# Performance work log

Measured on AMD Instinct MI355X. Metric: run time of the kernel, lower is better.

## Reference

```python
import jax, jax.numpy as jnp
import numpy as np

N = 20000        # nodes
E = 320000       # edges (avg degree 16)
G = 128          # graphs in batch
D_IN = 128
H = 128          # hidden_dim
HEADS = 8
OUT = 2
BN_EPS = 1e-5


def _segment_softmax(logits, seg, num_segments):
    # numerically stable softmax over segments along leading dim
    m = jax.ops.segment_max(logits, seg, num_segments)
    e = jnp.exp(logits - m[seg])
    s = jax.ops.segment_sum(e, seg, num_segments)
    return e / (s[seg] + 1e-16)


def _forward(x, gin1_w1, gin1_b1, gin1_w2, gin1_b2,
             gin2_w1, gin2_b1, gin2_w2, gin2_b2,
             gin3_w1, gin3_b1, gin3_w2, gin3_b2,
             gin4_w1, gin4_b1, gin4_w2, gin4_b2,
             bn1_g, bn1_b, bn2_g, bn2_b, bn3_g, bn3_b, bn4_g, bn4_b, bn5_g, bn5_b,
             gat_w, gat_asrc, gat_adst, gat_bias,
             gate_w, gate_b, fc1_w, fc1_b, fc2_w, fc2_b,
             edge_index, batch):
    src, dst = edge_index[0], edge_index[1]

    def gin(h, w1, b1, w2, b2):
        # GINConv, eps=0: mlp(x + sum_{j->i} x_j)
        agg = jax.ops.segment_sum(h[src], dst, N)
        z = agg + h
        return jax.nn.relu(z @ w1 + b1) @ w2 + b2

    def bn(h, g, b):
        # BatchNorm1d with batch statistics (training-mode normalization)
        mu = h.mean(0)
        var = ((h - mu) ** 2).mean(0)
        return g * (h - mu) * jax.lax.rsqrt(var + BN_EPS) + b

    # dropout is identity at inference
    h = jax.nn.relu(bn(gin(x, gin1_w1, gin1_b1, gin1_w2, gin1_b2), bn1_g, bn1_b))
    h = jax.nn.relu(bn(gin(h, gin2_w1, gin2_b1, gin2_w2, gin2_b2), bn2_g, bn2_b))
    h = jax.nn.relu(bn(gin(h, gin3_w1, gin3_b1, gin3_w2, gin3_b2), bn3_g, bn3_b))
    h = jax.nn.relu(bn(gin(h, gin4_w1, gin4_b1, gin4_w2, gin4_b2), bn4_g, bn4_b))

    # GATConv(2H -> H, heads=HEADS, concat=False) with self-loops (PyG default)
    loop = jnp.arange(N)
    s = jnp.concatenate([src, loop])
    d = jnp.concatenate([dst, loop])
    xh = (h @ gat_w).reshape(N, HEADS, H)                     # [N, heads, H]
    a_s = jnp.einsum('nhc,hc->nh', xh, gat_asrc)              # [N, heads]
    a_d = jnp.einsum('nhc,hc->nh', xh, gat_adst)
    e = jax.nn.leaky_relu(a_s[s] + a_d[d], 0.2)               # [E+N, heads]
    alpha = _segment_softmax(e, d, N)                         # softmax over in-edges of dst
    out = jax.ops.segment_sum(alpha[:, :, None] * xh[s], d, N)  # [N, heads, H]
    h = out.mean(1) + gat_bias                                # concat=False -> mean heads
    h = jax.nn.relu(bn(h, bn5_g, bn5_b))

    # GlobalAttention pooling: softmax(gate_nn(x)) per graph, weighted sum
    gate_logit = (h @ gate_w + gate_b)[:, 0]                  # [N]
    gate = _segment_softmax(gate_logit, batch, G)
    pooled = jax.ops.segment_sum(gate[:, None] * h, batch, G)  # [G, H]

    return jax.nn.relu(pooled @ fc1_w + fc1_b) @ fc2_w + fc2_b  # [G, OUT]


def setup_inputs() -> dict:
    key = jax.random.key(0)
    kit = iter(jax.random.split(key, 64))

    def nrm(shape, s=0.05):
        return jax.random.normal(next(kit), shape, jnp.float32) * s

    inp = {}
    inp['x'] = jax.random.normal(next(kit), (N, D_IN), jnp.float32)
    inp['edge_index'] = jax.random.randint(next(kit), (2, E), 0, N)
    inp['batch'] = jnp.sort(jax.random.randint(next(kit), (N,), 0, G))
    gin_dims = [(D_IN, H), (H, 2 * H), (2 * H, 4 * H), (4 * H, 2 * H)]
    for i, (a, b) in enumerate(gin_dims, 1):
        inp[f'gin{i}_w1'] = nrm((a, b))
        inp[f'gin{i}_b1'] = jnp.zeros((b,), jnp.float32)
        inp[f'gin{i}_w2'] = nrm((b, b))
        inp[f'gin{i}_b2'] = jnp.zeros((b,), jnp.float32)
    for i, dd in enumerate([H, 2 * H, 4 * H, 2 * H, H], 1):
        inp[f'bn{i}_g'] = jnp.ones((dd,), jnp.float32)
        inp[f'bn{i}_b'] = jnp.zeros((dd,), jnp.float32)
    inp['gat_w'] = nrm((2 * H, HEADS * H))
    inp['gat_asrc'] = nrm((HEADS, H))
    inp['gat_adst'] = nrm((HEADS, H))
    inp['gat_bias'] = jnp.zeros((H,), jnp.float32)
    inp['gate_w'] = nrm((H, 1))
    inp['gate_b'] = jnp.zeros((1,), jnp.float32)
    inp['fc1_w'] = nrm((H, 128))
    inp['fc1_b'] = jnp.zeros((128,), jnp.float32)
    inp['fc2_w'] = nrm((128, OUT))
    inp['fc2_b'] = jnp.zeros((OUT,), jnp.float32)
    return inp


def reference(x, edge_index, batch,
              gin1_w1, gin1_b1, gin1_w2, gin1_b2,
              gin2_w1, gin2_b1, gin2_w2, gin2_b2,
              gin3_w1, gin3_b1, gin3_w2, gin3_b2,
              gin4_w1, gin4_b1, gin4_w2, gin4_b2,
              bn1_g, bn1_b, bn2_g, bn2_b, bn3_g, bn3_b, bn4_g, bn4_b, bn5_g, bn5_b,
              gat_w, gat_asrc, gat_adst, gat_bias,
              gate_w, gate_b, fc1_w, fc1_b, fc2_w, fc2_b):
    return _forward(x, gin1_w1, gin1_b1, gin1_w2, gin1_b2,
                    gin2_w1, gin2_b1, gin2_w2, gin2_b2,
                    gin3_w1, gin3_b1, gin3_w2, gin3_b2,
                    gin4_w1, gin4_b1, gin4_w2, gin4_b2,
                    bn1_g, bn1_b, bn2_g, bn2_b, bn3_g, bn3_b, bn4_g, bn4_b, bn5_g, bn5_b,
                    gat_w, gat_asrc, gat_adst, gat_bias,
                    gate_w, gate_b, fc1_w, fc1_b, fc2_w, fc2_b,
                    edge_index, batch)
```

## Files before the change

kernel.cpp:

```cpp
#include <hip/hip_runtime.h>
#include <hip/hip_bf16.h>
#include <math.h>

#define NN 20000
#define NE 320000
#define NG 128

using bf16x8 = __attribute__((ext_vector_type(8))) short;
using f32x4  = __attribute__((ext_vector_type(4))) float;

static __device__ __forceinline__ float lrelu(float v){ return v > 0.f ? v : 0.2f*v; }
static __device__ __forceinline__ float b2f(unsigned short u){ unsigned int v = ((unsigned int)u) << 16; return __uint_as_float(v); }
static __device__ __forceinline__ unsigned short f2b(float f){
  unsigned int x = __float_as_uint(f);
  unsigned int r = x + 0x7fffu + ((x >> 16) & 1u);
  return (unsigned short)(r >> 16);
}
static __device__ __forceinline__ void gl16(const unsigned short* g, unsigned short* l){
  __builtin_amdgcn_global_load_lds((const __attribute__((address_space(1))) void*)g,
                                   (__attribute__((address_space(3))) void*)l, 16, 0, 0);
}
static __device__ __forceinline__ uint4 bn8(uint4 u, const float* scs, const float* shs, int f0){
  float v[8] = { b2f(u.x & 0xffff), b2f(u.x >> 16), b2f(u.y & 0xffff), b2f(u.y >> 16),
                 b2f(u.z & 0xffff), b2f(u.z >> 16), b2f(u.w & 0xffff), b2f(u.w >> 16) };
// ... 59 lines not shown
  }
}

struct WPrep {
  const float* W[9];
  unsigned short* Wt[9];
  int K[9];
  int Nn[9];
  int tileStart[10];
  const float* x;
  unsigned int* xb;
};

__global__ __launch_bounds__(256)
void k_prep2(WPrep P){
  __shared__ float tile[64][65];
  int b = blockIdx.x;
  if (b < P.tileStart[9]){
    int i = 0;
    while (i < 8 && b >= P.tileStart[i+1]) i++;
    int ti = b - P.tileStart[i];
    int K = P.K[i], Nn = P.Nn[i];
    int ntc = Nn >> 6;
    int k0 = (ti / ntc) << 6, n0 = (ti % ntc) << 6;
    int c = threadIdx.x & 63, ro = threadIdx.x >> 6;
    const float* W = P.W[i];
    #pragma unroll
    for (int rr = 0; rr < 16; rr++){
      int r = rr*4 + ro;
      tile[c][r] = W[(size_t)(k0 + r)*Nn + n0 + c];
    }
    __syncthreads();
    unsigned short* Wt = P.Wt[i];
    #pragma unroll
    for (int cc = 0; cc < 16; cc++){
      int cidx = cc*4 + ro;
      Wt[(size_t)(n0 + cidx)*K + k0 + c] = f2b(tile[cidx][c]);
    }
  } else {
    int idx = (b - P.tileStart[9])*256 + threadIdx.x;
    if (idx < NN*64){
      unsigned int lo = f2b(P.x[2*idx]);
      unsigned int hi = f2b(P.x[2*idx + 1]);
      P.xb[idx] = lo | (hi << 16);
    }
  }
}

template<int MODE, int DU>
__global__ __launch_bounds__(256)
void k_agg(const unsigned int* __restrict__ hU, const int* __restrict__ ptr,
           const int* __restrict__ csrc, unsigned int* __restrict__ z,
           const double* __restrict__ stats, const float* __restrict__ g,
           const float* __restrict__ bb, const float* __restrict__ bias){
  const int d = DU*2;
  __shared__ float scs[MODE == 1 ? 512 : 1];
  __shared__ float shs[MODE == 1 ? 512 : 1];
  int t = threadIdx.x;
  if (MODE == 1){
    for (int f = t; f < d; f += 256){
      double inv = 1.0 / (double)NN;
      double mu  = stats[f]*inv;
      double var = stats[d + f]*inv - mu*mu;
      if (var < 0.0) var = 0.0;
      float sc = g[f] * rsqrtf((float)var + 1e-5f);
      scs[f] = sc;
      shs[f] = bb[f] - (float)mu*sc;
    }
    __syncthreads();
  }
  const int npb = 256/DU;
  int n  = blockIdx.x*npb + t/DU;
  int tl = t & (DU - 1);
  int f0 = 2*tl, f1 = f0 + 1;
  float sc0 = 0.f, sh0 = 0.f, sc1 = 0.f, sh1 = 0.f;
  if (MODE == 1){ sc0 = scs[f0]; sh0 = shs[f0]; sc1 = scs[f1]; sh1 = shs[f1]; }
  int beg = ptr[n], deg = ptr[n+1] - beg;
  unsigned int self = hU[(size_t)n*DU + tl];
  float a0, a1;
// ... 7 lines not shown
  int i = 0;
  for (; i + 8 <= deg; i += 8){
    unsigned int v[8];
    #pragma unroll
    for (int u = 0; u < 8; u++) v[u] = hU[(size_t)csrc[beg + i + u]*DU + tl];
    #pragma unroll
    for (int u = 0; u < 8; u++){
      if (MODE == 1){
        a0 += fmaxf(b2f(v[u] & 0xffff)*sc0 + sh0, 0.f);
        a1 += fmaxf(b2f(v[u] >> 16)   *sc1 + sh1, 0.f);
      } else {
        a0 += b2f(v[u] & 0xffff);
        a1 += b2f(v[u] >> 16);
      }
    }
  }
  for (; i < deg; i++){
    unsigned int v = hU[(size_t)csrc[beg + i]*DU + tl];
    if (MODE == 1){
      a0 += fmaxf(b2f(v & 0xffff)*sc0 + sh0, 0.f);
      a1 += fmaxf(b2f(v >> 16)   *sc1 + sh1, 0.f);
    } else {
      a0 += b2f(v & 0xffff);
      a1 += b2f(v >> 16);
    }
  }
  if (MODE == 2){
    a0 = fmaxf(a0 + bias[f0], 0.f);
    a1 = fmaxf(a1 + bias[f1], 0.f);
  }
  z[(size_t)n*DU + tl] = (unsigned int)f2b(a0) | ((unsigned int)f2b(a1) << 16);
}

template<int ACT, int OBF, int STATS, int SCORES, int BNA>
__global__ __launch_bounds__(256)
void k_gemm_mfma(const unsigned short* __restrict__ A, const unsigned short* __restrict__ Bt,
                 const float* __restrict__ bias, float* __restrict__ C,
                 unsigned short* __restrict__ Cb, double* __restrict__ stats,
                 const float* __restrict__ asrc, const float* __restrict__ adst,
                 float* __restrict__ a_s, float* __restrict__ a_d,
                 const double* __restrict__ bnst, const float* __restrict__ bng,
                 const float* __restrict__ bnb,
                 int M, int Nn, int K){
  const int LDA = BNA ? 40 : 32;
  __shared__ unsigned short As[2][128*(BNA ? 40 : 32)];
  __shared__ unsigned short Bs[2][128*32];
  __shared__ float sS[SCORES ? 128 : 1];
  __shared__ float sD[SCORES ? 128 : 1];
  __shared__ float scs[BNA ? 512 : 1];
  __shared__ float shs[BNA ? 512 : 1];
  const int bm = blockIdx.y*128, bn = blockIdx.x*128;
  const int tid = threadIdx.x;
  const int lane = tid & 63;
  const int wave = tid >> 6;
  const int wm = (wave >> 1)*64, wn = (wave & 1)*64;
  const int lr = lane & 15, lq = lane >> 4;

  f32x4 acc[4][4];
  #pragma unroll
  for (int i = 0; i < 4; i++)
    #pragma unroll
    for (int j = 0; j < 4; j++) acc[i][j] = (f32x4){0.f,0.f,0.f,0.f};

  const int rowA = tid >> 2, q = tid & 3;
  const int ldsOff = wave*16*32;
  const int gmA0 = min(bm + rowA,      M-1);
  const int gmA1 = min(bm + rowA + 64, M-1);
  const unsigned short* pA0 = &A[(size_t)gmA0*K + q*8];
  const unsigned short* pA1 = &A[(size_t)gmA1*K + q*8];
  const unsigned short* pB0 = &Bt[(size_t)(bn + rowA)*K + q*8];
  const unsigned short* pB1 = &Bt[(size_t)(bn + rowA + 64)*K + q*8];

  if (BNA){
    for (int f = tid; f < K; f += 256){
      double inv = 1.0 / (double)NN;
      double mu  = bnst[f]*inv;
      double var = bnst[K + f]*inv - mu*mu;
      if (var < 0.0) var = 0.0;
      float sc = bng[f] * rsqrtf((float)var + 1e-5f);
      scs[f] = sc;
      shs[f] = bnb[f] - (float)mu*sc;
// ... 33 lines not shown
    bf16x8 af[4], bf[4];
    #pragma unroll
    for (int mi = 0; mi < 4; mi++)
      af[mi] = *(const bf16x8*)&As[cur][(wm + mi*16 + lr)*LDA + lq*8];
    #pragma unroll
    for (int ni = 0; ni < 4; ni++)
      bf[ni] = *(const bf16x8*)&Bs[cur][(wn + ni*16 + lr)*32 + lq*8];
    #pragma unroll
    for (int mi = 0; mi < 4; mi++)
      #pragma unroll
      for (int ni = 0; ni < 4; ni++)
        acc[mi][ni] = __builtin_amdgcn_mfma_f32_16x16x32_bf16(af[mi], bf[ni], acc[mi][ni], 0, 0, 0);
    if (BNA && kn < K){
      int f0 = kn + q*8;
      *(uint4*)&As[cur^1][ rowA      *LDA + q*8] = bn8(nu0, scs, shs, f0);
      *(uint4*)&As[cur^1][(rowA + 64)*LDA + q*8] = bn8(nu1, scs, shs, f0);
    }
    __syncthreads();
    cur ^= 1;
  }

  float cs[4] = {0.f,0.f,0.f,0.f}, cq[4] = {0.f,0.f,0.f,0.f};
  #pragma unroll
  for (int mi = 0; mi < 4; mi++){
    #pragma unroll
    for (int j = 0; j < 4; j++){
      int gm = bm + wm + mi*16 + lq*4 + j;
      if (gm < M){
        #pragma unroll
        for (int ni = 0; ni < 4; ni++){
          int gn = bn + wn + ni*16 + lr;
          float v = acc[mi][ni][j] + (bias ? bias[gn] : 0.f);
          if (ACT) v = fmaxf(v, 0.f);
          if (OBF) Cb[(size_t)gm*Nn + gn] = f2b(v);
          else     C [(size_t)gm*Nn + gn] = v;
          if (STATS){ cs[ni] += v; cq[ni] += v*v; }
        }
      }
    }
  }
  if (STATS){
    #pragma unroll
    for (int ni = 0; ni < 4; ni++){
      float s = cs[ni], qq = cq[ni];
      s += __shfl_xor(s, 16); s += __shfl_xor(s, 32);
      qq += __shfl_xor(qq, 16); qq += __shfl_xor(qq, 32);
      if (lane < 16){
        int gn = bn + wn + ni*16 + lr;
        atomicAdd(&stats[gn],      (double)s);
        atomicAdd(&stats[Nn + gn], (double)qq);
      }
    }
  }
  if (SCORES){
    const int hd = bn >> 7;
    float av[4], dv[4];
    #pragma unroll
    for (int ni = 0; ni < 4; ni++){
      int c = wn + ni*16 + lr;
      av[ni] = asrc[hd*128 + c];
      dv[ni] = adst[hd*128 + c];
    }
    float psS[4][4], psD[4][4];
    #pragma unroll
    for (int mi = 0; mi < 4; mi++)
      #pragma unroll
      for (int j = 0; j < 4; j++){
        float s = 0.f, d2 = 0.f;
        #pragma unroll
        for (int ni = 0; ni < 4; ni++){
          float v = acc[mi][ni][j];
          s  += v*av[ni];
          d2 += v*dv[ni];
        }
        #pragma unroll
        for (int o = 1; o < 16; o <<= 1){ s += __shfl_xor(s, o); d2 += __shfl_xor(d2, o); }
        psS[mi][j] = s; psD[mi][j] = d2;
      }
    if (wn == 0 && lr == 0){
      #pragma unroll
      for (int mi = 0; mi < 4; mi++)
        #pragma unroll
        for (int j = 0; j < 4; j++){
          int r = wm + mi*16 + lq*4 + j;
          sS[r] = psS[mi][j]; sD[r] = psD[mi][j];
        }
    }
    __syncthreads();
    if (wn != 0 && lr == 0){
      #pragma unroll
      for (int mi = 0; mi < 4; mi++)
        #pragma unroll
        for (int j = 0; j < 4; j++){
          int r = wm + mi*16 + lq*4 + j;
          sS[r] += psS[mi][j]; sD[r] += psD[mi][j];
        }
    }
    __syncthreads();
    if (tid < 128){
      int gm = bm + tid;
      if (gm < M){ a_s[gm*8 + hd] = sS[tid]; a_d[gm*8 + hd] = sD[tid]; }
    }
  }
}

__global__ __launch_bounds__(256)
void k_gin1_mlp(const unsigned short* __restrict__ Z, const unsigned short* __restrict__ W1t,
                const float* __restrict__ b1, const unsigned short* __restrict__ W2t,
                const float* __restrict__ b2, unsigned short* __restrict__ Out,
                double* __restrict__ stats, int M){
  __shared__ unsigned short As[2][128*32];
  __shared__ unsigned short Bs[2][128*32];
  __shared__ unsigned short hid[128*136];
  const int bm = blockIdx.x*128;
  const int tid = threadIdx.x;
  const int lane = tid & 63;
  const int wave = tid >> 6;
  const int wm = (wave >> 1)*64, wn = (wave & 1)*64;
  const int lr = lane & 15, lq = lane >> 4;
  const int rowA = tid >> 2, q = tid & 3;
  const int ldsOff = wave*16*32;
  const int gm0 = min(bm + rowA,      M-1);
  const int gm1 = min(bm + rowA + 64, M-1);
  const unsigned short* pA0 = &Z[(size_t)gm0*128 + q*8];
  const unsigned short* pA1 = &Z[(size_t)gm1*128 + q*8];
  const unsigned short* pB0 = &W1t[(size_t)rowA*128 + q*8];
  const unsigned short* pB1 = &W1t[(size_t)(rowA + 64)*128 + q*8];

  f32x4 acc[4][4];
  #pragma unroll
  for (int i = 0; i < 4; i++)
    #pragma unroll
    for (int j = 0; j < 4; j++) acc[i][j] = (f32x4){0.f,0.f,0.f,0.f};

// ... 76 lines not shown
    __syncthreads();
    cur ^= 1;
  }
  float cs[4] = {0.f,0.f,0.f,0.f}, cq[4] = {0.f,0.f,0.f,0.f};
  #pragma unroll
  for (int mi = 0; mi < 4; mi++){
    #pragma unroll
    for (int j = 0; j < 4; j++){
      int gm = bm + wm + mi*16 + lq*4 + j;
      if (gm < M){
        #pragma unroll
        for (int ni = 0; ni < 4; ni++){
          int gn = wn + ni*16 + lr;
          float v = acc2[mi][ni][j] + b2[gn];
          Out[(size_t)gm*128 + gn] = f2b(v);
          cs[ni] += v; cq[ni] += v*v;
        }
      }
    }
  }
  #pragma unroll
  for (int ni = 0; ni < 4; ni++){
    float s = cs[ni], qq = cq[ni];
    s += __shfl_xor(s, 16); s += __shfl_xor(s, 32);
    qq += __shfl_xor(qq, 16); qq += __shfl_xor(qq, 32);
    if (lane < 16){
      int gn = wn + ni*16 + lr;
      atomicAdd(&stats[gn],       (double)s);
      atomicAdd(&stats[128 + gn], (double)qq);
    }
  }
}

__global__ void k_bn_stats16(const unsigned short* __restrict__ h, int d, double* __restrict__ stats){
  int r0 = blockIdx.x*64;
  int rend = min(NN, r0 + 64);
  for (int f = threadIdx.x; f < d; f += blockDim.x){
    float s = 0.f, q = 0.f;
    for (int r = r0; r < rend; r++){ float v = b2f(h[(size_t)r*d + f]); s += v; q += v*v; }
    atomicAdd(&stats[f], (double)s);
    atomicAdd(&stats[d + f], (double)q);
  }
}

__global__ __launch_bounds__(256)
void k_bn_relu_gate(const unsigned short* __restrict__ hpre, unsigned short* __restrict__ hb,
                    int total8, const double* __restrict__ stats,
                    const float* __restrict__ g, const float* __restrict__ b,
                    const float* __restrict__ gatew, const float* __restrict__ gateb,
                    float* __restrict__ logit){
  const int d = 128;
  __shared__ float scs[128], shs[128];
  for (int f = threadIdx.x; f < d; f += blockDim.x){
    double inv = 1.0 / (double)NN;
    double mu  = stats[f]*inv;
    double var = stats[d + f]*inv - mu*mu;
    if (var < 0.0) var = 0.0;
    float sc = g[f] * rsqrtf((float)var + 1e-5f);
    scs[f] = sc;
    shs[f] = b[f] - (float)mu*sc;
  }
  __syncthreads();
  int i = blockIdx.x*blockDim.x + threadIdx.x;
  if (i >= total8) return;
  int i8 = i*8;
  uint4 u = *(const uint4*)&hpre[i8];
  float v[8] = { b2f(u.x & 0xffff), b2f(u.x >> 16), b2f(u.y & 0xffff), b2f(u.y >> 16),
                 b2f(u.z & 0xffff), b2f(u.z >> 16), b2f(u.w & 0xffff), b2f(u.w >> 16) };
  int f0 = i8 & 127;
  float gp = 0.f;
  #pragma unroll
  for (int j = 0; j < 8; j++){
    float y = fmaxf(v[j]*scs[f0 + j] + shs[f0 + j], 0.f);
    v[j] = y;
    gp += y*gatew[f0 + j];
  }
  uint4 p;
  p.x = (unsigned int)f2b(v[0]) | ((unsigned int)f2b(v[1]) << 16);
  p.y = (unsigned int)f2b(v[2]) | ((unsigned int)f2b(v[3]) << 16);
  p.z = (unsigned int)f2b(v[4]) | ((unsigned int)f2b(v[5]) << 16);
  p.w = (unsigned int)f2b(v[6]) | ((unsigned int)f2b(v[7]) << 16);
  *(uint4*)&hb[i8] = p;
  #pragma unroll
  for (int o = 1; o < 16; o <<= 1) gp += __shfl_xor(gp, o);
  if ((threadIdx.x & 15) == 0) logit[i >> 4] = gp + gateb[0];
}

__global__ __launch_bounds__(256)
void k_gat_node256(const unsigned short* __restrict__ xh, const float* __restrict__ a_s,
                   const float* __restrict__ a_d, const int* __restrict__ ptr,
                   const int* __restrict__ csrc, const float* __restrict__ bias,
                   unsigned short* __restrict__ hout){
  int n = blockIdx.x, t = threadIdx.x;
  int beg = ptr[n], deg = ptr[n+1] - beg;
  int tot = deg + 1;
  __shared__ float elv[256][9];
  __shared__ int esrc[256];
  __shared__ float red[256];
  __shared__ float ms[8], ssinv[8], adn[8];
  __shared__ float partial[16][132];
  if (t < 8) adn[t] = a_d[n*8 + t];
  __syncthreads();
  int head = t >> 5, slot = t & 31;
  int sub = t >> 7, tt = t & 127;
  int h16 = tt >> 4;
  float acc[8] = {0.f,0.f,0.f,0.f,0.f,0.f,0.f,0.f};

  if (tot <= 256){
    for (int i = t; i < tot; i += 256) esrc[i] = (i < deg) ? csrc[beg + i] : n;
    __syncthreads();
    for (int i = t; i < tot*8; i += 256){
      int le = i >> 3, hh = i & 7;
      elv[le][hh] = lrelu(a_s[esrc[le]*8 + hh] + adn[hh]);
    }
    __syncthreads();
    float mx = -1e30f;
    for (int e = slot; e < tot; e += 32) mx = fmaxf(mx, elv[e][head]);
    red[t] = mx; __syncthreads();
    #pragma unroll
    for (int off = 16; off >= 1; off >>= 1){
      if (slot < off) red[t] = fmaxf(red[t], red[t + off]);
      __syncthreads();
    }
    if (slot == 0) ms[head] = red[t];
    __syncthreads();
    float sm = 0.f;
    for (int e = slot; e < tot; e += 32){
      float ex = __expf(elv[e][head] - ms[head]);
      elv[e][head] = ex;
      sm += ex;
    }
    red[t] = sm; __syncthreads();
    #pragma unroll
    for (int off = 16; off >= 1; off >>= 1){
      if (slot < off) red[t] += red[t + off];
      __syncthreads();
    }
    if (slot == 0) ssinv[head] = 1.f / (red[t] + 1e-16f);
    __syncthreads();
    int lo = sub*128, hi = min(tot, lo + 128);
    float si = ssinv[h16];
    int i = lo;
    for (; i + 2 <= hi; i += 2){
      const uint4* r0 = (const uint4*)(xh + (size_t)esrc[i]*1024);
      const uint4* r1 = (const uint4*)(xh + (size_t)esrc[i+1]*1024);
      uint4 v0 = r0[tt], v1 = r1[tt];
      float a0 = elv[i][h16]*si, a1 = elv[i+1][h16]*si;
      acc[0] += a0*b2f(v0.x & 0xffff) + a1*b2f(v1.x & 0xffff);
      acc[1] += a0*b2f(v0.x >> 16)    + a1*b2f(v1.x >> 16);
      acc[2] += a0*b2f(v0.y & 0xffff) + a1*b2f(v1.y & 0xffff);
      acc[3] += a0*b2f(v0.y >> 16)    + a1*b2f(v1.y >> 16);
      acc[4] += a0*b2f(v0.z & 0xffff) + a1*b2f(v1.z & 0xffff);
      acc[5] += a0*b2f(v0.z >> 16)    + a1*b2f(v1.z >> 16);
      acc[6] += a0*b2f(v0.w & 0xffff) + a1*b2f(v1.w & 0xffff);
      acc[7] += a0*b2f(v0.w >> 16)    + a1*b2f(v1.w >> 16);
    }
    for (; i < hi; i++){
      const uint4* r0 = (const uint4*)(xh + (size_t)esrc[i]*1024);
      uint4 v0 = r0[tt];
      float a0 = elv[i][h16]*si;
      acc[0] += a0*b2f(v0.x & 0xffff); acc[1] += a0*b2f(v0.x >> 16);
      acc[2] += a0*b2f(v0.y & 0xffff); acc[3] += a0*b2f(v0.y >> 16);
      acc[4] += a0*b2f(v0.z & 0xffff); acc[5] += a0*b2f(v0.z >> 16);
      acc[6] += a0*b2f(v0.w & 0xffff); acc[7] += a0*b2f(v0.w >> 16);
    }
    __syncthreads();
  } else {
    float mx = -1e30f;
    for (int e = slot; e < tot; e += 32){
      int s = (e < deg) ? csrc[beg + e] : n;
      mx = fmaxf(mx, lrelu(a_s[s*8 + head] + adn[head]));
    }
    red[t] = mx; __syncthreads();
    #pragma unroll
    for (int off = 16; off >= 1; off >>= 1){
      if (slot < off) red[t] = fmaxf(red[t], red[t + off]);
      __syncthreads();
    }
    if (slot == 0) ms[head] = red[t];
    __syncthreads();
    float sm = 0.f;
    for (int e = slot; e < tot; e += 32){
      int s = (e < deg) ? csrc[beg + e] : n;
      sm += __expf(lrelu(a_s[s*8 + head] + adn[head]) - ms[head]);
    }
    red[t] = sm; __syncthreads();
    #pragma unroll
    for (int off = 16; off >= 1; off >>= 1){
      if (slot < off) red[t] += red[t + off];
      __syncthreads();
    }
    if (slot == 0) ssinv[head] = 1.f / (red[t] + 1e-16f);
    __syncthreads();
    float si = ssinv[h16];
    for (int ch = 0; ch < tot; ch += 256){
      int ce = min(256, tot - ch);
      for (int i = t; i < ce*8; i += 256){
        int le = i >> 3, hh = i & 7;
        int s = (ch + le < deg) ? csrc[beg + ch + le] : n;
        if (hh == 0) esrc[le] = s;
        elv[le][hh] = __expf(lrelu(a_s[s*8 + hh] + adn[hh]) - ms[hh]);
      }
      __syncthreads();
      int lo = sub*128, hi = min(ce, lo + 128);
      for (int i = lo; i < hi; i++){
        const uint4* r0 = (const uint4*)(xh + (size_t)esrc[i]*1024);
        uint4 v0 = r0[tt];
        float a0 = elv[i][h16]*si;
        acc[0] += a0*b2f(v0.x & 0xffff); acc[1] += a0*b2f(v0.x >> 16);
        acc[2] += a0*b2f(v0.y & 0xffff); acc[3] += a0*b2f(v0.y >> 16);
        acc[4] += a0*b2f(v0.z & 0xffff); acc[5] += a0*b2f(v0.z >> 16);
        acc[6] += a0*b2f(v0.w & 0xffff); acc[7] += a0*b2f(v0.w >> 16);
      }
      __syncthreads();
    }
  }

  int c0 = (tt & 15)*8;
  #pragma unroll
  for (int j = 0; j < 8; j++) partial[sub*8 + h16][c0 + j] = acc[j];
  __syncthreads();
  if (t < 128){
    float s = 0.f;
    #pragma unroll
    for (int g = 0; g < 16; g++) s += partial[g][t];
    hout[(size_t)n*128 + t] = f2b(s*0.125f + bias[t]);
  }
}

__global__ void k_poolhead(const unsigned short* __restrict__ h, const float* __restrict__ logit,
                           const int* __restrict__ gptr,
                           const float* __restrict__ w1, const float* __restrict__ b1,
                           const float* __restrict__ w2, const float* __restrict__ b2,
                           float* __restrict__ out){
  int g = blockIdx.x, t = threadIdx.x;
  int beg = gptr[g], end = gptr[g+1];
  __shared__ float red[128];
  __shared__ float prow[128];
  __shared__ float r1[128];
  __shared__ float m_sh, s_sh;
  float mx = -1e30f;
  for (int i = beg + t; i < end; i += 128) mx = fmaxf(mx, logit[i]);
  red[t] = mx; __syncthreads();
  for (int off = 64; off > 0; off >>= 1){ if (t < off) red[t] = fmaxf(red[t], red[t + off]); __syncthreads(); }
  if (t == 0) m_sh = red[0];
  __syncthreads();
  float sm = 0.f;
  for (int i = beg + t; i < end; i += 128) sm += __expf(logit[i] - m_sh);
  red[t] = sm; __syncthreads();
  for (int off = 64; off > 0; off >>= 1){ if (t < off) red[t] += red[t + off]; __syncthreads(); }
  if (t == 0) s_sh = red[0] + 1e-16f;
  __syncthreads();
  float acc = 0.f;
  for (int i = beg; i < end; i++){
    float w = __expf(logit[i] - m_sh) / s_sh;
    acc += w * b2f(h[(size_t)i*128 + t]);
  }
  prow[t] = acc;
  __syncthreads();
  float a = b1[t];
// ... 11 lines not shown
extern "C" void kernel_launch(void* const* d_in, const int* in_sizes, int n_in,
                              void* d_out, int out_size, void* d_ws, size_t ws_size,
                              hipStream_t stream) {
  const float* x        = (const float*)d_in[0];
  const int*   ei       = (const int*)  d_in[1];
  const int*   batch    = (const int*)  d_in[2];
  const float* gw1[4] = {(const float*)d_in[3],  (const float*)d_in[7],  (const float*)d_in[11], (const float*)d_in[15]};
  const float* gb1[4] = {(const float*)d_in[4],  (const float*)d_in[8],  (const float*)d_in[12], (const float*)d_in[16]};
  const float* gw2[4] = {(const float*)d_in[5],  (const float*)d_in[9],  (const float*)d_in[13], (const float*)d_in[17]};
  const float* gb2[4] = {(const float*)d_in[6],  (const float*)d_in[10], (const float*)d_in[14], (const float*)d_in[18]};
  const float* bng[5] = {(const float*)d_in[19], (const float*)d_in[21], (const float*)d_in[23], (const float*)d_in[25], (const float*)d_in[27]};
  const float* bnb[5] = {(const float*)d_in[20], (const float*)d_in[22], (const float*)d_in[24], (const float*)d_in[26], (const float*)d_in[28]};
  const float* gat_w    = (const float*)d_in[29];
  const float* gat_asrc = (const float*)d_in[30];
  const float* gat_adst = (const float*)d_in[31];
  const float* gat_bias = (const float*)d_in[32];
  const float* gate_w   = (const float*)d_in[33];
  const float* gate_b   = (const float*)d_in[34];
  const float* fc1_w    = (const float*)d_in[35];
  const float* fc1_b    = (const float*)d_in[36];
  const float* fc2_w    = (const float*)d_in[37];
  const float* fc2_b    = (const float*)d_in[38];
  const int* src = ei;
  const int* dst = ei + NE;

  char* wsb = (char*)d_ws;
  size_t off = 0;
  auto take = [&](size_t bytes) -> void* {
    void* p = wsb + off;
    off = (off + bytes + 255) & ~(size_t)255;
    return p;
  };
  unsigned short* hpre  = (unsigned short*)take((size_t)NN*512*2);
  unsigned short* hb    = (unsigned short*)take((size_t)NN*512*2);
  unsigned short* zh    = (unsigned short*)take((size_t)NN*1024*2);
  unsigned short* z16   = zh;
  unsigned short* hid16 = zh + (size_t)NN*512;
  unsigned short* xh16  = zh;
  unsigned short* xb    = (unsigned short*)take((size_t)NN*128*2);
  unsigned short* wt    = (unsigned short*)take((size_t)1000000*2);
  int*    deg    = (int*)   take((size_t)NN*4);
  int*    cnt    = (int*)   take((size_t)NN*4);
  int*    gdeg   = (int*)   take((size_t)NG*4);
  double* statsA = (double*)take(2560*8);
  float*  a_s    = (float*) take((size_t)NN*8*4);
  float*  a_d    = (float*) take((size_t)NN*8*4);
  float*  logit  = (float*) take((size_t)NN*4);
  int*    rowptr = (int*)   take((size_t)(NN+1)*4);
  int*    gptr   = (int*)   take((size_t)(NG+1)*4);
  int*    csrc   = (int*)   take((size_t)NE*4);
  (void)ws_size; (void)n_in; (void)in_sizes; (void)out_size;

  unsigned short* wt_g1w1 = wt;
  unsigned short* wt_g1w2 = wt_g1w1 + 128*128;
  unsigned short* wt_g2w1 = wt_g1w2 + 128*128;
  unsigned short* wt_g2w2 = wt_g2w1 + 256*128;
  unsigned short* wt_g3w1 = wt_g2w2 + 256*256;
  unsigned short* wt_g3w2 = wt_g3w1 + 512*256;
  unsigned short* wt_g4w1 = wt_g3w2 + 512*512;
  unsigned short* wt_g4w2 = wt_g4w1 + 256*512;
  unsigned short* wt_gat  = wt_g4w2 + 256*256;

  double* st1 = statsA + 0;
  double* st2 = statsA + 256;
  double* st3 = statsA + 768;
  double* st4 = statsA + 1792;
  double* st5 = statsA + 2304;

  hipMemsetAsync(deg, 0, (size_t)((char*)(statsA + 2560) - (char*)deg), stream);

  k_hist2<<<(NE + NN + 255)/256, 256, 0, stream>>>(dst, batch, deg, gdeg);
  k_scan2<<<2, 1024, 0, stream>>>(deg, rowptr, gdeg, gptr);
  k_fill<<<(NE + 255)/256, 256, 0, stream>>>(src, dst, rowptr, cnt, csrc);

  {
    WPrep P;
    const float* Ws[9] = {gw1[0], gw2[0], gw1[1], gw2[1], gw1[2], gw2[2], gw1[3], gw2[3], gat_w};
    unsigned short* Wts[9] = {wt_g1w1, wt_g1w2, wt_g2w1, wt_g2w2, wt_g3w1, wt_g3w2, wt_g4w1, wt_g4w2, wt_gat};
    int Ks[9]  = {128, 128, 128, 256, 256, 512, 512, 256, 256};
    int Nns[9] = {128, 128, 256, 256, 512, 512, 256, 256, 1024};
    int cum = 0;
    for (int i = 0; i < 9; i++){
      P.W[i] = Ws[i]; P.Wt[i] = Wts[i]; P.K[i] = Ks[i]; P.Nn[i] = Nns[i];
      P.tileStart[i] = cum;
      cum += (Ks[i] >> 6)*(Nns[i] >> 6);
    }
    P.tileStart[9] = cum;
    P.x = x; P.xb = (unsigned int*)xb;
    int xblocks = (NN*64 + 255)/256;
    k_prep2<<<cum + xblocks, 256, 0, stream>>>(P);
  }

  const int GM = (NN + 127) / 128;
  #define NP9 nullptr, nullptr, nullptr, nullptr
  #define NB3 nullptr, nullptr, nullptr

  k_agg<0,64><<<NN/4, 256, 0, stream>>>((const unsigned int*)xb, rowptr, csrc, (unsigned int*)z16, nullptr, nullptr, nullptr, nullptr);
  k_gin1_mlp<<<GM, 256, 0, stream>>>(z16, wt_g1w1, gb1[0], wt_g1w2, gb2[0], hpre, st1, NN);

  k_agg<1,64><<<NN/4, 256, 0, stream>>>((const unsigned int*)hpre, rowptr, csrc, (unsigned int*)z16, st1, bng[0], bnb[0], nullptr);
  k_gemm_mfma<1,1,0,0,0><<<dim3(2, GM), 256, 0, stream>>>(z16, wt_g2w1, gb1[1], nullptr, hid16, nullptr, NP9, NB3, NN, 256, 128);
  k_gemm_mfma<0,1,1,0,0><<<dim3(2, GM), 256, 0, stream>>>(hid16, wt_g2w2, gb2[1], nullptr, hpre, st2, NP9, NB3, NN, 256, 256);

  k_agg<1,128><<<NN/2, 256, 0, stream>>>((const unsigned int*)hpre, rowptr, csrc, (unsigned int*)z16, st2, bng[1], bnb[1], nullptr);
  k_gemm_mfma<1,1,0,0,0><<<dim3(4, GM), 256, 0, stream>>>(z16, wt_g3w1, gb1[2], nullptr, hid16, nullptr, NP9, NB3, NN, 512, 256);
  k_gemm_mfma<0,1,1,0,0><<<dim3(4, GM), 256, 0, stream>>>(hid16, wt_g3w2, gb2[2], nullptr, hpre, st3, NP9, NB3, NN, 512, 512);

  k_gemm_mfma<0,1,0,0,1><<<dim3(2, GM), 256, 0, stream>>>(hpre, wt_g4w1, nullptr, nullptr, hid16, nullptr, NP9, st3, bng[2], bnb[2], NN, 256, 512);
  k_agg<2,128><<<NN/2, 256, 0, stream>>>((const unsigned int*)hid16, rowptr, csrc, (unsigned int*)z16, nullptr, nullptr, nullptr, gb1[3]);
  k_gemm_mfma<0,1,1,0,0><<<dim3(2, GM), 256, 0, stream>>>(z16, wt_g4w2, gb2[3], nullptr, hpre, st4, NP9, NB3, NN, 256, 256);

  k_gemm_mfma<0,1,0,1,1><<<dim3(8, GM), 256, 0, stream>>>(hpre, wt_gat, nullptr, nullptr, xh16, nullptr, gat_asrc, gat_adst, a_s, a_d, st4, bng[3], bnb[3], NN, 1024, 256);
  k_gat_node256<<<NN, 256, 0, stream>>>(xh16, a_s, a_d, rowptr, csrc, gat_bias, hpre);
  k_bn_stats16<<<(NN + 63)/64, 128, 0, stream>>>(hpre, 128, st5);
  k_bn_relu_gate<<<(NN*128/8 + 255)/256, 256, 0, stream>>>(hpre, hb, NN*128/8, st5, bng[4], bnb[4], gate_w, gate_b, logit);

  k_poolhead<<<NG, 128, 0, stream>>>(hb, logit, gptr, fc1_w, fc1_b, fc2_w, fc2_b, (float*)d_out);
}
```

Measured before the change: 601.0 us.

## Reorder GAT to aggregate inputs before projection, folding attention vectors into weights

Attention scores are now computed from a small GEMM of the BN-applied input against precomputed W·a_src/W·a_dst vectors. The softmax-weighted aggregation then runs over the 256-wide input features per head. Only after that does one GEMM with a head-stacked, 1/8-scaled weight (K=2048) produce the 128-wide output, with BN stats fused into its epilogue. This avoids writing and gathering the N×1024 projected features and removes the separate BN stats kernel. In exchange the aggregation kernel writes a 2048-wide bf16 buffer per node and does 16 accumulators per thread, so memory traffic moves rather than disappearing.

Measured after the change: 617.4 us. 1.03x slower.

```diff
diff --git a/kernel.cpp b/kernel.cpp
--- a/kernel.cpp
+++ b/kernel.cpp
@@ -115,10 +115,19 @@
     }
     __syncthreads();
     unsigned short* Wt = P.Wt[i];
-    #pragma unroll
-    for (int cc = 0; cc < 16; cc++){
-      int cidx = cc*4 + ro;
-      Wt[(size_t)(n0 + cidx)*K + k0 + c] = f2b(tile[cidx][c]);
+    if (i == 8){
+      int hh = n0 >> 7, cl0 = n0 & 127;
+      #pragma unroll
+      for (int cc = 0; cc < 16; cc++){
+        int cidx = cc*4 + ro;
+        Wt[(size_t)(cl0 + cidx)*2048 + hh*256 + k0 + c] = f2b(tile[cidx][c]*0.125f);
+      }
+    } else {
+      #pragma unroll
+      for (int cc = 0; cc < 16; cc++){
+        int cidx = cc*4 + ro;
+        Wt[(size_t)(n0 + cidx)*K + k0 + c] = f2b(tile[cidx][c]);
+      }
     }
   } else {
     int idx = (b - P.tileStart[9])*256 + threadIdx.x;
@@ -128,6 +137,21 @@
       P.xb[idx] = lo | (hi << 16);
     }
   }
+}
+
+__global__ void k_wasd(const float* __restrict__ W, const float* __restrict__ asrc,
+                       const float* __restrict__ adst, unsigned short* __restrict__ Bt_sc){
+  __shared__ float av[128];
+  int b = blockIdx.x;
+  int h = b & 7, isd = b >> 3;
+  int k = threadIdx.x;
+  if (k < 128) av[k] = (isd ? adst : asrc)[h*128 + k];
+  __syncthreads();
+  const float* Wr = W + (size_t)k*1024 + h*128;
+  float s = 0.f;
+  #pragma unroll 8
+  for (int c = 0; c < 128; c++) s += Wr[c]*av[c];
+  Bt_sc[b*256 + k] = f2b(s);
 }
 
 template<int MODE, int DU>
@@ -201,21 +225,17 @@
   z[(size_t)n*DU + tl] = (unsigned int)f2b(a0) | ((unsigned int)f2b(a1) << 16);
 }
 
-template<int ACT, int OBF, int STATS, int SCORES, int BNA>
+template<int ACT, int OBF, int STATS, int PK, int BNA>
 __global__ __launch_bounds__(256)
 void k_gemm_mfma(const unsigned short* __restrict__ A, const unsigned short* __restrict__ Bt,
                  const float* __restrict__ bias, float* __restrict__ C,
                  unsigned short* __restrict__ Cb, double* __restrict__ stats,
-                 const float* __restrict__ asrc, const float* __restrict__ adst,
-                 float* __restrict__ a_s, float* __restrict__ a_d,
                  const double* __restrict__ bnst, const float* __restrict__ bng,
                  const float* __restrict__ bnb,
                  int M, int Nn, int K){
   const int LDA = BNA ? 40 : 32;
   __shared__ unsigned short As[2][128*(BNA ? 40 : 32)];
   __shared__ unsigned short Bs[2][128*32];
-  __shared__ float sS[SCORES ? 128 : 1];
-  __shared__ float sD[SCORES ? 128 : 1];
   __shared__ float scs[BNA ? 512 : 1];
   __shared__ float shs[BNA ? 512 : 1];
   const int bm = blockIdx.y*128, bn = blockIdx.x*128;
@@ -315,7 +335,8 @@
           int gn = bn + wn + ni*16 + lr;
           float v = acc[mi][ni][j] + (bias ? bias[gn] : 0.f);
           if (ACT) v = fmaxf(v, 0.f);
-          if (OBF) Cb[(size_t)gm*Nn + gn] = f2b(v);
+          if (PK){ if (gn < 16) C[(size_t)gm*16 + gn] = v; }
+          else if (OBF) Cb[(size_t)gm*Nn + gn] = f2b(v);
           else     C [(size_t)gm*Nn + gn] = v;
           if (STATS){ cs[ni] += v; cq[ni] += v*v; }
         }
@@ -333,56 +354,6 @@
         atomicAdd(&stats[gn],      (double)s);
         atomicAdd(&stats[Nn + gn], (double)qq);
       }
-    }
-  }
-  if (SCORES){
-    const int hd = bn >> 7;
-    float av[4], dv[4];
-    #pragma unroll
-    for (int ni = 0; ni < 4; ni++){
-      int c = wn + ni*16 + lr;
-      av[ni] = asrc[hd*128 + c];
-      dv[ni] = adst[hd*128 + c];
-    }
-    float psS[4][4], psD[4][4];
-    #pragma unroll
-    for (int mi = 0; mi < 4; mi++)
-      #pragma unroll
-      for (int j = 0; j < 4; j++){
-        float s = 0.f, d2 = 0.f;
-        #pragma unroll
-        for (int ni = 0; ni < 4; ni++){
-          float v = acc[mi][ni][j];
-          s  += v*av[ni];
-          d2 += v*dv[ni];
-        }
-        #pragma unroll
-        for (int o = 1; o < 16; o <<= 1){ s += __shfl_xor(s, o); d2 += __shfl_xor(d2, o); }
-        psS[mi][j] = s; psD[mi][j] = d2;
-      }
-    if (wn == 0 && lr == 0){
-      #pragma unroll
-      for (int mi = 0; mi < 4; mi++)
-        #pragma unroll
-        for (int j = 0; j < 4; j++){
-          int r = wm + mi*16 + lq*4 + j;
-          sS[r] = psS[mi][j]; sD[r] = psD[mi][j];
-        }
-    }
-    __syncthreads();
-    if (wn != 0 && lr == 0){
-      #pragma unroll
-      for (int mi = 0; mi < 4; mi++)
-        #pragma unroll
-        for (int j = 0; j < 4; j++){
-          int r = wm + mi*16 + lq*4 + j;
-          sS[r] += psS[mi][j]; sD[r] += psD[mi][j];
-        }
-    }
-    __syncthreads();
-    if (tid < 128){
-      int gm = bm + tid;
-      if (gm < M){ a_s[gm*8 + hd] = sS[tid]; a_d[gm*8 + hd] = sD[tid]; }
     }
   }
 }
@@ -525,14 +496,144 @@
   }
 }
 
-__global__ void k_bn_stats16(const unsigned short* __restrict__ h, int d, double* __restrict__ stats){
-  int r0 = blockIdx.x*64;
-  int rend = min(NN, r0 + 64);
-  for (int f = threadIdx.x; f < d; f += blockDim.x){
-    float s = 0.f, q = 0.f;
-    for (int r = r0; r < rend; r++){ float v = b2f(h[(size_t)r*d + f]); s += v; q += v*v; }
-    atomicAdd(&stats[f], (double)s);
-    atomicAdd(&stats[d + f], (double)q);
+__global__ __launch_bounds__(256)
+void k_gat_agg(const unsigned int* __restrict__ hU, const float* __restrict__ a_sd,
+               const int* __restrict__ ptr, const int* __restrict__ csrc,
+               const double* __restrict__ st, const float* __restrict__ g,
+               const float* __restrict__ bb, unsigned int* __restrict__ agg){
+  int n = blockIdx.x, t = threadIdx.x;
+  __shared__ float scs[256], shs[256];
+  __shared__ float elv[256][9];
+  __shared__ int esrc[256];
+  __shared__ float red[256];
+  __shared__ float ms[8], ssinv[8], adn[8];
+  __shared__ float partial[2][8][260];
+  {
+    int f = t;
+    double inv = 1.0/(double)NN;
+    double mu = st[f]*inv;
+    double var = st[256 + f]*inv - mu*mu;
+    if (var < 0.0) var = 0.0;
+    float sc = g[f]*rsqrtf((float)var + 1e-5f);
+    scs[f] = sc; shs[f] = bb[f] - (float)mu*sc;
+  }
+  if (t < 8) adn[t] = a_sd[n*16 + 8 + t];
+  __syncthreads();
+  int beg = ptr[n], deg = ptr[n+1] - beg, tot = deg + 1;
+  int head = t >> 5, slot = t & 31;
+  int grp = t >> 7, l = t & 127;
+  float sc0 = scs[2*l], sh0 = shs[2*l], sc1 = scs[2*l+1], sh1 = shs[2*l+1];
+  float acc[16];
+  #pragma unroll
+  for (int j = 0; j < 16; j++) acc[j] = 0.f;
+
+  if (tot <= 256){
+    for (int i = t; i < tot; i += 256) esrc[i] = (i < deg) ? csrc[beg + i] : n;
+    __syncthreads();
+    for (int i = t; i < tot*8; i += 256){
+      int le = i >> 3, hh = i & 7;
+      elv[le][hh] = lrelu(a_sd[esrc[le]*16 + hh] + adn[hh]);
+    }
+    __syncthreads();
+    float mx = -1e30f;
+    for (int e = slot; e < tot; e += 32) mx = fmaxf(mx, elv[e][head]);
+    red[t] = mx; __syncthreads();
+    #pragma unroll
+    for (int off = 16; off >= 1; off >>= 1){
+      if (slot < off) red[t] = fmaxf(red[t], red[t + off]);
+      __syncthreads();
+    }
+    if (slot == 0) ms[head] = red[t];
+    __syncthreads();
+    float sm = 0.f;
+    for (int e = slot; e < tot; e += 32){
+      float ex = __expf(elv[e][head] - ms[head]);
+      elv[e][head] = ex;
+      sm += ex;
+    }
+    red[t] = sm; __syncthreads();
+    #pragma unroll
+    for (int off = 16; off >= 1; off >>= 1){
+      if (slot < off) red[t] += red[t + off];
+      __syncthreads();
+    }
+    if (slot == 0) ssinv[head] = 1.f / (red[t] + 1e-16f);
+    __syncthreads();
+    for (int e = grp; e < tot; e += 2){
+      unsigned int u = hU[(size_t)esrc[e]*128 + l];
+      float v0 = fmaxf(b2f(u & 0xffff)*sc0 + sh0, 0.f);
+      float v1 = fmaxf(b2f(u >> 16)   *sc1 + sh1, 0.f);
+      #pragma unroll
+      for (int h = 0; h < 8; h++){
+        float a = elv[e][h];
+        acc[2*h]   += a*v0;
+        acc[2*h+1] += a*v1;
+      }
+    }
+    __syncthreads();
+  } else {
+    float mx = -1e30f;
+    for (int e = slot; e < tot; e += 32){
+      int s = (e < deg) ? csrc[beg + e] : n;
+      mx = fmaxf(mx, lrelu(a_sd[s*16 + head] + adn[head]));
+    }
+    red[t] = mx; __syncthreads();
+    #pragma unroll
+    for (int off = 16; off >= 1; off >>= 1){
+      if (slot < off) red[t] = fmaxf(red[t], red[t + off]);
+      __syncthreads();
+    }
+    if (slot == 0) ms[head] = red[t];
+    __syncthreads();
+    float sm = 0.f;
+    for (int e = slot; e < tot; e += 32){
+      int s = (e < deg) ? csrc[beg + e] : n;
+      sm += __expf(lrelu(a_sd[s*16 + head] + adn[head]) - ms[head]);
+    }
+    red[t] = sm; __syncthreads();
+    #pragma unroll
+    for (int off = 16; off >= 1; off >>= 1){
+      if (slot < off) red[t] += red[t + off];
+      __syncthreads();
+    }
+    if (slot == 0) ssinv[head] = 1.f / (red[t] + 1e-16f);
+    __syncthreads();
+    for (int c0 = 0; c0 < tot; c0 += 256){
+      int ce = min(256, tot - c0);
+      for (int i = t; i < ce*8; i += 256){
+        int le = i >> 3, hh = i & 7;
+        int s = (c0 + le < deg) ? csrc[beg + c0 + le] : n;
+        if (hh == 0) esrc[le] = s;
+        elv[le][hh] = __expf(lrelu(a_sd[s*16 + hh] + adn[hh]) - ms[hh]);
+      }
+      __syncthreads();
+      for (int e = grp; e < ce; e += 2){
+        unsigned int u = hU[(size_t)esrc[e]*128 + l];
+        float v0 = fmaxf(b2f(u & 0xffff)*sc0 + sh0, 0.f);
+        float v1 = fmaxf(b2f(u >> 16)   *sc1 + sh1, 0.f);
+        #pragma unroll
+        for (int h = 0; h < 8; h++){
+          float a = elv[e][h];
+          acc[2*h]   += a*v0;
+          acc[2*h+1] += a*v1;
+        }
+      }
+      __syncthreads();
+    }
+  }
+
+  #pragma unroll
+  for (int h = 0; h < 8; h++){
+    partial[grp][h][2*l]   = acc[2*h];
+    partial[grp][h][2*l+1] = acc[2*h+1];
+  }
+  __syncthreads();
+  for (int o = t; o < 1024; o += 256){
+    int h = o >> 7, k2 = (o & 127)*2;
+    float si = ssinv[h];
+    float w0 = (partial[0][h][k2]     + partial[1][h][k2])    *si;
+    float w1 = (partial[0][h][k2 + 1] + partial[1][h][k2 + 1])*si;
+    agg[(size_t)n*1024 + o] = (unsigned int)f2b(w0) | ((unsigned int)f2b(w1) << 16);
   }
 }
 
@@ -577,148 +678,6 @@
   #pragma unroll
   for (int o = 1; o < 16; o <<= 1) gp += __shfl_xor(gp, o);
   if ((threadIdx.x & 15) == 0) logit[i >> 4] = gp + gateb[0];
-}
-
-__global__ __launch_bounds__(256)
-void k_gat_node256(const unsigned short* __restrict__ xh, const float* __restrict__ a_s,
-                   const float* __restrict__ a_d, const int* __restrict__ ptr,
-                   const int* __restrict__ csrc, const float* __restrict__ bias,
-                   unsigned short* __restrict__ hout){
-  int n = blockIdx.x, t = threadIdx.x;
-  int beg = ptr[n], deg = ptr[n+1] - beg;
-  int tot = deg + 1;
-  __shared__ float elv[256][9];
-  __shared__ int esrc[256];
-  __shared__ float red[256];
-  __shared__ float ms[8], ssinv[8], adn[8];
-  __shared__ float partial[16][132];
-  if (t < 8) adn[t] = a_d[n*8 + t];
-  __syncthreads();
-  int head = t >> 5, slot = t & 31;
-  int sub = t >> 7, tt = t & 127;
-  int h16 = tt >> 4;
-  float acc[8] = {0.f,0.f,0.f,0.f,0.f,0.f,0.f,0.f};
-
-  if (tot <= 256){
-    for (int i = t; i < tot; i += 256) esrc[i] = (i < deg) ? csrc[beg + i] : n;
-    __syncthreads();
-    for (int i = t; i < tot*8; i += 256){
-      int le = i >> 3, hh = i & 7;
-      elv[le][hh] = lrelu(a_s[esrc[le]*8 + hh] + adn[hh]);
-    }
-    __syncthreads();
-    float mx = -1e30f;
-    for (int e = slot; e < tot; e += 32) mx = fmaxf(mx, elv[e][head]);
-    red[t] = mx; __syncthreads();
-    #pragma unroll
-    for (int off = 16; off >= 1; off >>= 1){
-      if (slot < off) red[t] = fmaxf(red[t], red[t + off]);
-      __syncthreads();
-    }
-    if (slot == 0) ms[head] = red[t];
-    __syncthreads();
-    float sm = 0.f;
-    for (int e = slot; e < tot; e += 32){
-      float ex = __expf(elv[e][head] - ms[head]);
-      elv[e][head] = ex;
-      sm += ex;
-    }
-    red[t] = sm; __syncthreads();
-    #pragma unroll
-    for (int off = 16; off >= 1; off >>= 1){
-      if (slot < off) red[t] += red[t + off];
-      __syncthreads();
-    }
-    if (slot == 0) ssinv[head] = 1.f / (red[t] + 1e-16f);
-    __syncthreads();
-    int lo = sub*128, hi = min(tot, lo + 128);
-    float si = ssinv[h16];
-    int i = lo;
-    for (; i + 2 <= hi; i += 2){
-      const uint4* r0 = (const uint4*)(xh + (size_t)esrc[i]*1024);
-      const uint4* r1 = (const uint4*)(xh + (size_t)esrc[i+1]*1024);
-      uint4 v0 = r0[tt], v1 = r1[tt];
-      float a0 = elv[i][h16]*si, a1 = elv[i+1][h16]*si;
-      acc[0] += a0*b2f(v0.x & 0xffff) + a1*b2f(v1.x & 0xffff);
-      acc[1] += a0*b2f(v0.x >> 16)    + a1*b2f(v1.x >> 16);
-      acc[2] += a0*b2f(v0.y & 0xffff) + a1*b2f(v1.y & 0xffff);
-      acc[3] += a0*b2f(v0.y >> 16)    + a1*b2f(v1.y >> 16);
-      acc[4] += a0*b2f(v0.z & 0xffff) + a1*b2f(v1.z & 0xffff);
-      acc[5] += a0*b2f(v0.z >> 16)    + a1*b2f(v1.z >> 16);
-      acc[6] += a0*b2f(v0.w & 0xffff) + a1*b2f(v1.w & 0xffff);
-      acc[7] += a0*b2f(v0.w >> 16)    + a1*b2f(v1.w >> 16);
-    }
-    for (; i < hi; i++){
-      const uint4* r0 = (const uint4*)(xh + (size_t)esrc[i]*1024);
-      uint4 v0 = r0[tt];
-      float a0 = elv[i][h16]*si;
-      acc[0] += a0*b2f(v0.x & 0xffff); acc[1] += a0*b2f(v0.x >> 16);
-      acc[2] += a0*b2f(v0.y & 0xffff); acc[3] += a0*b2f(v0.y >> 16);
-      acc[4] += a0*b2f(v0.z & 0xffff); acc[5] += a0*b2f(v0.z >> 16);
-      acc[6] += a0*b2f(v0.w & 0xffff); acc[7] += a0*b2f(v0.w >> 16);
-    }
-    __syncthreads();
-  } else {
-    float mx = -1e30f;
-    for (int e = slot; e < tot; e += 32){
-      int s = (e < deg) ? csrc[beg + e] : n;
-      mx = fmaxf(mx, lrelu(a_s[s*8 + head] + adn[head]));
-    }
-    red[t] = mx; __syncthreads();
-    #pragma unroll
-    for (int off = 16; off >= 1; off >>= 1){
-      if (slot < off) red[t] = fmaxf(red[t], red[t + off]);
-      __syncthreads();
-    }
-    if (slot == 0) ms[head] = red[t];
-    __syncthreads();
-    float sm = 0.f;
-    for (int e = slot; e < tot; e += 32){
-      int s = (e < deg) ? csrc[beg + e] : n;
-      sm += __expf(lrelu(a_s[s*8 + head] + adn[head]) - ms[head]);
-    }
-    red[t] = sm; __syncthreads();
-    #pragma unroll
-    for (int off = 16; off >= 1; off >>= 1){
-      if (slot < off) red[t] += red[t + off];
-      __syncthreads();
-    }
-    if (slot == 0) ssinv[head] = 1.f / (red[t] + 1e-16f);
-    __syncthreads();
-    float si = ssinv[h16];
-    for (int ch = 0; ch < tot; ch += 256){
-      int ce = min(256, tot - ch);
-      for (int i = t; i < ce*8; i += 256){
-        int le = i >> 3, hh = i & 7;
-        int s = (ch + le < deg) ? csrc[beg + ch + le] : n;
-        if (hh == 0) esrc[le] = s;
-        elv[le][hh] = __expf(lrelu(a_s[s*8 + hh] + adn[hh]) - ms[hh]);
-      }
-      __syncthreads();
-      int lo = sub*128, hi = min(ce, lo + 128);
-      for (int i = lo; i < hi; i++){
-        const uint4* r0 = (const uint4*)(xh + (size_t)esrc[i]*1024);
-        uint4 v0 = r0[tt];
-        float a0 = elv[i][h16]*si;
-        acc[0] += a0*b2f(v0.x & 0xffff); acc[1] += a0*b2f(v0.x >> 16);
-        acc[2] += a0*b2f(v0.y & 0xffff); acc[3] += a0*b2f(v0.y >> 16);
-        acc[4] += a0*b2f(v0.z & 0xffff); acc[5] += a0*b2f(v0.z >> 16);
-        acc[6] += a0*b2f(v0.w & 0xffff); acc[7] += a0*b2f(v0.w >> 16);
-      }
-      __syncthreads();
-    }
-  }
-
-  int c0 = (tt & 15)*8;
-  #pragma unroll
-  for (int j = 0; j < 8; j++) partial[sub*8 + h16][c0 + j] = acc[j];
-  __syncthreads();
-  if (t < 128){
-    float s = 0.f;
-    #pragma unroll
-    for (int g = 0; g < 16; g++) s += partial[g][t];
-    hout[(size_t)n*128 + t] = f2b(s*0.125f + bias[t]);
-  }
 }
 
 __global__ void k_poolhead(const unsigned short* __restrict__ h, const float* __restrict__ logit,
@@ -796,19 +755,19 @@
     return p;
   };
   unsigned short* hpre  = (unsigned short*)take((size_t)NN*512*2);
-  unsigned short* hb    = (unsigned short*)take((size_t)NN*512*2);
-  unsigned short* zh    = (unsigned short*)take((size_t)NN*1024*2);
-  unsigned short* z16   = zh;
-  unsigned short* hid16 = zh + (size_t)NN*512;
-  unsigned short* xh16  = zh;
+  unsigned short* hb    = (unsigned short*)take((size_t)NN*128*2);
+  unsigned short* R     = (unsigned short*)take((size_t)NN*2048*2);
+  unsigned short* z16   = R;
+  unsigned short* hid16 = R + (size_t)NN*512;
+  unsigned short* agg16 = R;
   unsigned short* xb    = (unsigned short*)take((size_t)NN*128*2);
   unsigned short* wt    = (unsigned short*)take((size_t)1000000*2);
   int*    deg    = (int*)   take((size_t)NN*4);
   int*    cnt    = (int*)   take((size_t)NN*4);
   int*    gdeg   = (int*)   take((size_t)NG*4);
   double* statsA = (double*)take(2560*8);
-  float*  a_s    = (float*) take((size_t)NN*8*4);
-  float*  a_d    = (float*) take((size_t)NN*8*4);
+  unsigned short* Bt_sc = (unsigned short*)take((size_t)128*256*2);
+  float*  a_sd   = (float*) take((size_t)NN*16*4);
   float*  logit  = (float*) take((size_t)NN*4);
   int*    rowptr = (int*)   take((size_t)(NN+1)*4);
   int*    gptr   = (int*)   take((size_t)(NG+1)*4);
@@ -823,7 +782,7 @@
   unsigned short* wt_g3w2 = wt_g3w1 + 512*256;
   unsigned short* wt_g4w1 = wt_g3w2 + 512*512;
   unsigned short* wt_g4w2 = wt_g4w1 + 256*512;
-  unsigned short* wt_gat  = wt_g4w2 + 256*256;
+  unsigned short* wt_gat2 = wt_g4w2 + 256*256;
 
   double* st1 = statsA + 0;
   double* st2 = statsA + 256;
@@ -831,7 +790,7 @@
   double* st4 = statsA + 1792;
   double* st5 = statsA + 2304;
 
-  hipMemsetAsync(deg, 0, (size_t)((char*)(statsA + 2560) - (char*)deg), stream);
+  hipMemsetAsync(deg, 0, (size_t)((char*)(Bt_sc + 128*256) - (char*)deg), stream);
 
   k_hist2<<<(NE + NN + 255)/256, 256, 0, stream>>>(dst, batch, deg, gdeg);
   k_scan2<<<2, 1024, 0, stream>>>(deg, rowptr, gdeg, gptr);
@@ -840,7 +799,7 @@
   {
     WPrep P;
     const float* Ws[9] = {gw1[0], gw2[0], gw1[1], gw2[1], gw1[2], gw2[2], gw1[3], gw2[3], gat_w};
-    unsigned short* Wts[9] = {wt_g1w1, wt_g1w2, wt_g2w1, wt_g2w2, wt_g3w1, wt_g3w2, wt_g4w1, wt_g4w2, wt_gat};
+    unsigned short* Wts[9] = {wt_g1w1, wt_g1w2, wt_g2w1, wt_g2w2, wt_g3w1, wt_g3w2, wt_g4w1, wt_g4w2, wt_gat2};
     int Ks[9]  = {128, 128, 128, 256, 256, 512, 512, 256, 256};
     int Nns[9] = {128, 128, 256, 256, 512, 512, 256, 256, 1024};
     int cum = 0;
@@ -854,30 +813,30 @@
     int xblocks = (NN*64 + 255)/256;
     k_prep2<<<cum + xblocks, 256, 0, stream>>>(P);
   }
+  k_wasd<<<16, 256, 0, stream>>>(gat_w, gat_asrc, gat_adst, Bt_sc);
 
   const int GM = (NN + 127) / 128;
-  #define NP9 nullptr, nullptr, nullptr, nullptr
   #define NB3 nullptr, nullptr, nullptr
 
   k_agg<0,64><<<NN/4, 256, 0, stream>>>((const unsigned int*)xb, rowptr, csrc, (unsigned int*)z16, nullptr, nullptr, nullptr, nullptr);
   k_gin1_mlp<<<GM, 256, 0, stream>>>(z16, wt_g1w1, gb1[0], wt_g1w2, gb2[0], hpre, st1, NN);
 
   k_agg<1,64><<<NN/4, 256, 0, stream>>>((const unsigned int*)hpre, rowptr, csrc, (unsigned int*)z16, st1, bng[0], bnb[0], nullptr);
-  k_gemm_mfma<1,1,0,0,0><<<dim3(2, GM), 256, 0, stream>>>(z16, wt_g2w1, gb1[1], nullptr, hid16, nullptr, NP9, NB3, NN, 256, 128);
-  k_gemm_mfma<0,1,1,0,0><<<dim3(2, GM), 256, 0, stream>>>(hid16, wt_g2w2, gb2[1], nullptr, hpre, st2, NP9, NB3, NN, 256, 256);
+  k_gemm_mfma<1,1,0,0,0><<<dim3(2, GM), 256, 0, stream>>>(z16, wt_g2w1, gb1[1], nullptr, hid16, nullptr, NB3, NN, 256, 128);
+  k_gemm_mfma<0,1,1,0,0><<<dim3(2, GM), 256, 0, stream>>>(hid16, wt_g2w2, gb2[1], nullptr, hpre, st2, NB3, NN, 256, 256);
 
   k_agg<1,128><<<NN/2, 256, 0, stream>>>((const unsigned int*)hpre, rowptr, csrc, (unsigned int*)z16, st2, bng[1], bnb[1], nullptr);
-  k_gemm_mfma<1,1,0,0,0><<<dim3(4, GM), 256, 0, stream>>>(z16, wt_g3w1, gb1[2], nullptr, hid16, nullptr, NP9, NB3, NN, 512, 256);
-  k_gemm_mfma<0,1,1,0,0><<<dim3(4, GM), 256, 0, stream>>>(hid16, wt_g3w2, gb2[2], nullptr, hpre, st3, NP9, NB3, NN, 512, 512);
-
-  k_gemm_mfma<0,1,0,0,1><<<dim3(2, GM), 256, 0, stream>>>(hpre, wt_g4w1, nullptr, nullptr, hid16, nullptr, NP9, st3, bng[2], bnb[2], NN, 256, 512);
+  k_gemm_mfma<1,1,0,0,0><<<dim3(4, GM), 256, 0, stream>>>(z16, wt_g3w1, gb1[2], nullptr, hid16, nullptr, NB3, NN, 512, 256);
+  k_gemm_mfma<0,1,1,0,0><<<dim3(4, GM), 256, 0, stream>>>(hid16, wt_g3w2, gb2[2], nullptr, hpre, st3, NB3, NN, 512, 512);
+
+  k_gemm_mfma<0,1,0,0,1><<<dim3(2, GM), 256, 0, stream>>>(hpre, wt_g4w1, nullptr, nullptr, hid16, nullptr, st3, bng[2], bnb[2], NN, 256, 512);
   k_agg<2,128><<<NN/2, 256, 0, stream>>>((const unsigned int*)hid16, rowptr, csrc, (unsigned int*)z16, nullptr, nullptr, nullptr, gb1[3]);
-  k_gemm_mfma<0,1,1,0,0><<<dim3(2, GM), 256, 0, stream>>>(z16, wt_g4w2, gb2[3], nullptr, hpre, st4, NP9, NB3, NN, 256, 256);
-
-  k_gemm_mfma<0,1,0,1,1><<<dim3(8, GM), 256, 0, stream>>>(hpre, wt_gat, nullptr, nullptr, xh16, nullptr, gat_asrc, gat_adst, a_s, a_d, st4, bng[3], bnb[3], NN, 1024, 256);
-  k_gat_node256<<<NN, 256, 0, stream>>>(xh16, a_s, a_d, rowptr, csrc, gat_bias, hpre);
-  k_bn_stats16<<<(NN + 63)/64, 128, 0, stream>>>(hpre, 128, st5);
+  k_gemm_mfma<0,1,1,0,0><<<dim3(2, GM), 256, 0, stream>>>(z16, wt_g4w2, gb2[3], nullptr, hpre, st4, NB3, NN, 256, 256);
+
+  k_gemm_mfma<0,0,0,1,1><<<dim3(1, GM), 256, 0, stream>>>(hpre, Bt_sc, nullptr, a_sd, nullptr, nullptr, st4, bng[3], bnb[3], NN, 128, 256);
+  k_gat_agg<<<NN, 256, 0, stream>>>((const unsigned int*)hpre, a_sd, rowptr, csrc, st4, bng[3], bnb[3], (unsigned int*)agg16);
+  k_gemm_mfma<0,1,1,0,0><<<dim3(1, GM), 256, 0, stream>>>(agg16, wt_gat2, gat_bias, nullptr, hpre, st5, NB3, NN, 128, 2048);
+
   k_bn_relu_gate<<<(NN*128/8 + 255)/256, 256, 0, stream>>>(hpre, hb, NN*128/8, st5, bng[4], bnb[4], gate_w, gate_b, logit);
-
   k_poolhead<<<NG, 128, 0, stream>>>(hb, logit, gptr, fc1_w, fc1_b, fc2_w, fc2_b, (float*)d_out);
 }
```
